# Performance work log

Measured on AMD Instinct MI355X. Metric: run time of the kernel, lower is better.

The kernel has to match this reference:

```python
import jax, jax.numpy as jnp
import numpy as np

DEG20 = 20.0 * np.pi / 180.0
MIN_PATCH_AREA = 4.0


def _bilinear(p, sy, sx):
    """Bilinear sample [P,P,3] patch at float coords sy,sx of shape [H,W]."""
    P = p.shape[0]
    y0 = jnp.floor(sy)
    x0 = jnp.floor(sx)
    wy = (sy - y0)[..., None]
    wx = (sx - x0)[..., None]
    y0i = jnp.clip(y0, 0, P - 1).astype(jnp.int32)
    y1i = jnp.clip(y0 + 1, 0, P - 1).astype(jnp.int32)
    x0i = jnp.clip(x0, 0, P - 1).astype(jnp.int32)
    x1i = jnp.clip(x0 + 1, 0, P - 1).astype(jnp.int32)
    v00 = p[y0i, x0i]
    v01 = p[y0i, x1i]
    v10 = p[y1i, x0i]
    v11 = p[y1i, x1i]
    return v00 * (1 - wy) * (1 - wx) + v01 * (1 - wy) * wx + v10 * wy * (1 - wx) + v11 * wy * wx


def setup_inputs() -> dict:
    key = jax.random.key(0)
    B, H, W, N, P = 16, 768, 768, 16, 640
    k_img, k_patch, k_ymin, k_xmin, k_h, k_w = jax.random.split(key, 6)
    images = jax.random.uniform(k_img, (B, H, W, 3), jnp.float32, -1.0, 1.0)
    patch = jax.random.uniform(k_patch, (P, P, 3), jnp.float32, -1.0, 1.0)
    ymin = jax.random.uniform(k_ymin, (B, N), jnp.float32, 0.0, 0.55 * H)
    xmin = jax.random.uniform(k_xmin, (B, N), jnp.float32, 0.0, 0.55 * W)
    bh = jax.random.uniform(k_h, (B, N), jnp.float32, 60.0, 0.40 * H)
    bw = jax.random.uniform(k_w, (B, N), jnp.float32, 60.0, 0.40 * W)
    ymax = jnp.minimum(ymin + bh, float(H))
    xmax = jnp.minimum(xmin + bw, float(W))
    boxes = jnp.stack([ymin, xmin, ymax, xmax], axis=-1)  # [B,N,4]
    scale = jnp.float32(0.4)
    return {"images": images, "boxes": boxes, "patch": patch, "scale": scale}


def reference(images, boxes, patch, scale):
    B, H, W, _ = images.shape
    P = patch.shape[0]
    Hf, Wf = jnp.float32(H), jnp.float32(W)
    yy = jnp.arange(H, dtype=jnp.float32)[:, None]  # [H,1]
    xx = jnp.arange(W, dtype=jnp.float32)[None, :]  # [1,W]
    scale_s = jnp.reshape(scale, ())

    def per_image(img, bxs, ikey):
        kw, kb, kboxes = jax.random.split(ikey, 3)
        # random_print_adjust: w*patch + b, clipped
        wmul = 0.5 + 0.1 * jax.random.normal(kw, (1, 1, 3), jnp.float32)
        badd = 0.01 * jax.random.normal(kb, (1, 1, 3), jnp.float32)
        p = jnp.clip(wmul * patch + badd, -1.0, 1.0)
        # brightness matcher: shift patch mean toward image mean
        p = jnp.clip(p + (jnp.mean(img) - jnp.mean(p)), -1.0, 1.0)
        bkeys = jax.random.split(kboxes, bxs.shape[0])

        def step(im, inp):
            box, bk = inp
            k1, k2, k3, k4, k5 = jax.random.split(bk, 5)
            ymin, xmin, ymax, xmax = box[0], box[1], box[2], box[3]
            bh = ymax - ymin
            bw = xmax - xmin
            longer = jnp.maximum(bh, bw)
            psize = jnp.floor(longer * scale_s)            # patch_h == patch_w
            diag = jnp.minimum(jnp.float32(np.sqrt(2.0)) * psize, Wf)
            tol = 0.2
            oy = ymin + bh / 2 + jax.random.uniform(k1, (), jnp.float32, -tol * bh / 2, tol * bh / 2)
            ox = xmin + bw / 2 + jax.random.uniform(k2, (), jnp.float32, -tol * bw / 2, tol * bw / 2)
            y0 = jnp.maximum(oy - diag / 2, 0.0)
            x0 = jnp.maximum(ox - diag / 2, 0.0)
            y0 = jnp.where(y0 + diag > Hf, Hf - diag, y0)
            x0 = jnp.where(x0 + diag > Wf, Wf - diag, x0)
            # TF casts to int32 (truncation; values >= 0 -> floor)
            y0 = jnp.floor(y0)
            x0 = jnp.floor(x0)
            d = jnp.floor(diag)
            ph = psize
            valid = (ph * ph) > MIN_PATCH_AREA
            top = jnp.floor((d - ph) / 2.0)                # pad offset
            angle = jax.random.uniform(k3, (), jnp.float32, -DEG20, DEG20)
            # pixel coords inside the diag x diag patch window
            u = yy - y0                                    # [H,1] -> broadcast [H,W]
            v = xx - x0
            inside = (u >= 0) & (u < d) & (v >= 0) & (v < d)
            c = (d - 1.0) / 2.0
            ca, sa = jnp.cos(angle), jnp.sin(angle)
            iu = c + ca * (u - c) - sa * (v - c)           # inverse rotation about center
            iv = c + sa * (u - c) + ca * (v - c)
            py = iu - top                                  # coords in resized patch
            px = iv - top
            # bilinear resize (half-pixel centers): src = (dst+0.5)*P/ph - 0.5
            sy = (py + 0.5) * (P / ph) - 0.5
            sx = (px + 0.5) * (P / ph) - 0.5
            val = _bilinear(p, sy, sx)                     # [H,W,3]
            noise = jax.random.uniform(k4, (H, W, 3), jnp.float32, -0.01, 0.01)
            delta = jax.random.uniform(k5, (), jnp.float32, -0.3, 0.3)
            val = jnp.clip(val + noise + delta, -1.0, 1.0)
            in_patch = (py >= 0) & (py <= ph - 1) & (px >= 0) & (px <= ph - 1)
            fill = jnp.where(in_patch[..., None], val, -2.0)  # pad/rotate fill = -2
            blended = jnp.clip(jnp.where(fill < -1.0, im, fill), -1.0, 1.0)
            write = inside[..., None] & valid
            return jnp.where(write, blended, im), None

        out, _ = jax.lax.scan(step, img, (bxs, bkeys))
        return out

    ikeys = jax.random.split(jax.random.key(42), B)
    return jax.vmap(per_image)(images, boxes, ikeys)
```

## Files before the change

### kernel.cpp

```cpp
#include <hip/hip_runtime.h>
#include <stdint.h>

#define NIMG 16
#define IMH 768
#define IMW 768
#define NBOX 16
#define PSZ 640
#define IMG_ELEMS (IMH*IMW*3)
#define PATCH_ELEMS (PSZ*PSZ*3)
#define CPBLK 128
#define PATBLK 64
#define RENDER_BLKS 4096

typedef float f4 __attribute__((ext_vector_type(4)));

__device__ __forceinline__ uint32_t rotl32(uint32_t v, int r){ return (v<<r)|(v>>(32-r)); }

__device__ __forceinline__ void threefry(uint32_t k0, uint32_t k1, uint32_t c0, uint32_t c1,
                                         uint32_t& o0, uint32_t& o1){
  uint32_t ks2 = k0 ^ k1 ^ 0x1BD11BDAu;
  uint32_t x0 = c0 + k0, x1 = c1 + k1;
#define TFR(r) { x0 += x1; x1 = rotl32(x1,(r)); x1 ^= x0; }
  TFR(13) TFR(15) TFR(26) TFR(6)
  x0 += k1;  x1 += ks2 + 1u;
  TFR(17) TFR(29) TFR(16) TFR(24)
  x0 += ks2; x1 += k0 + 2u;
  TFR(13) TFR(15) TFR(26) TFR(6)
  x0 += k0;  x1 += k1 + 3u;
  TFR(17) TFR(29) TFR(16) TFR(24)
  x0 += k1;  x1 += ks2 + 4u;
  TFR(13) TFR(15) TFR(26) TFR(6)
  x0 += ks2; x1 += k0 + 5u;
#undef TFR
  o0 = x0; o1 = x1;
}

__device__ __forceinline__ uint32_t rbits(uint32_t k0, uint32_t k1, uint32_t idx){
  uint32_t a, b; threefry(k0, k1, 0u, idx, a, b); return a ^ b;
}

__device__ __forceinline__ float u01(uint32_t bits){
  return __uint_as_float((bits >> 9) | 0x3f800000u) - 1.0f;
}

__device__ __forceinline__ float juniform(uint32_t k0, uint32_t k1, uint32_t idx, float mn, float mx){
  float u = u01(rbits(k0, k1, idx));
  float span = __fsub_rn(mx, mn);
  return fmaxf(mn, __fadd_rn(__fmul_rn(u, span), mn));
}

__device__ float erfinv32(float x){
  float w = -log1pf(-x*x);
  float p;
  if (w < 5.0f){
    w = w - 2.5f;
    p = 2.81022636e-08f;
    p = fmaf(p,w, 3.43273939e-07f);
    p = fmaf(p,w,-3.5233877e-06f);
    p = fmaf(p,w,-4.39150654e-06f);
    p = fmaf(p,w, 0.00021858087f);
    p = fmaf(p,w,-0.00125372503f);
    p = fmaf(p,w,-0.00417768164f);
    p = fmaf(p,w, 0.246640727f);
    p = fmaf(p,w, 1.50140941f);
  } else {
    w = sqrtf(w) - 3.0f;
    p = -0.000200214257f;
    p = fmaf(p,w, 0.000100950558f);
    p = fmaf(p,w, 0.00134934322f);
    p = fmaf(p,w,-0.00367342844f);
    p = fmaf(p,w, 0.00573950773f);
    p = fmaf(p,w,-0.0076224613f);
    p = fmaf(p,w, 0.00943887047f);
    p = fmaf(p,w, 1.00167406f);
    p = fmaf(p,w, 2.83297682f);
  }
  return p * x;
}

__device__ __forceinline__ void compute_wb(int b, float* rec){
  uint32_t i0,i1; threefry(0u, 42u, 0u, (uint32_t)b, i0, i1);
  uint32_t kw0,kw1; threefry(i0, i1, 0u, 0u, kw0, kw1);
  uint32_t kb0,kb1; threefry(i0, i1, 0u, 1u, kb0, kb1);
  const float lo = -0.99999994f;
  const float span = __fsub_rn(1.0f, lo);
  const float sq2 = 1.4142135623730951f;
  for (int j = 0; j < 3; j++){
    float uw = u01(rbits(kw0, kw1, (uint32_t)j));
    float rw = fmaxf(lo, __fadd_rn(__fmul_rn(uw, span), lo));
    float nw = __fmul_rn(sq2, erfinv32(rw));
    rec[j] = __fadd_rn(0.5f, __fmul_rn(0.1f, nw));
    float ub = u01(rbits(kb0, kb1, (uint32_t)j));
    float rb = fmaxf(lo, __fadd_rn(__fmul_rn(ub, span), lo));
    float nb = __fmul_rn(sq2, erfinv32(rb));
    rec[3+j] = __fmul_rn(0.01f, nb);
  }
  rec[6] = 0.0f; rec[7] = 0.0f;
}

__global__ __launch_bounds__(256) void k_front(const float* __restrict__ img,
                                               const float* __restrict__ patch,
                                               float* __restrict__ out,
                                               double* __restrict__ imgpart,
                                               double* __restrict__ patpart){
  if (blockIdx.x < PATBLK){
    __shared__ float wl[NIMG*8];
    if (threadIdx.x < NIMG) compute_wb(threadIdx.x, &wl[threadIdx.x*8]);
    __syncthreads();
    double s[NIMG];
    #pragma unroll
    for (int im = 0; im < NIMG; im++) s[im] = 0.0;
    const f4* p4 = (const f4*)patch;
    const int N4 = PATCH_ELEMS/4;
    for (int i = blockIdx.x*256 + threadIdx.x; i < N4; i += PATBLK*256){
      f4 v = __builtin_nontemporal_load(p4 + i);
      int c = (i << 2) % 3;
      #pragma unroll
      for (int q = 0; q < 4; q++){
        float pv = v[q];
        #pragma unroll
        for (int im = 0; im < NIMG; im++){
          float t = __fadd_rn(__fmul_rn(wl[im*8 + c], pv), wl[im*8 + 3 + c]);
          t = fminf(fmaxf(t, -1.0f), 1.0f);
          s[im] += (double)t;
        }
        c = (c == 2) ? 0 : c + 1;
      }
    }
    #pragma unroll
    for (int im = 0; im < NIMG; im++)
      for (int o = 32; o > 0; o >>= 1) s[im] += __shfl_down(s[im], o);
    __shared__ double red[4][NIMG];
    if ((threadIdx.x & 63) == 0){
      int w = threadIdx.x >> 6;
      #pragma unroll
      for (int im = 0; im < NIMG; im++) red[w][im] = s[im];
    }
    __syncthreads();
    if (threadIdx.x < NIMG){
      double t = red[0][threadIdx.x] + red[1][threadIdx.x] + red[2][threadIdx.x] + red[3][threadIdx.x];
      patpart[threadIdx.x*PATBLK + blockIdx.x] = t;
    }
  } else {
    int bi = blockIdx.x - PATBLK;
    int b = bi >> 7;
    int j = bi & (CPBLK-1);
    const f4* src = (const f4*)(img + (size_t)b * IMG_ELEMS);
    f4* dst = (f4*)(out + (size_t)b * IMG_ELEMS);
    const int N4 = IMG_ELEMS/4;
    double s = 0.0;
    for (int i = j*256 + threadIdx.x; i < N4; i += CPBLK*256){
      f4 v = __builtin_nontemporal_load(src + i);
      __builtin_nontemporal_store(v, dst + i);
      s += (double)v.x; s += (double)v.y; s += (double)v.z; s += (double)v.w;
    }
    for (int o = 32; o > 0; o >>= 1) s += __shfl_down(s, o);
    __shared__ double sm[4];
    if ((threadIdx.x & 63) == 0) sm[threadIdx.x >> 6] = s;
    __syncthreads();
    if (threadIdx.x == 0) imgpart[b*CPBLK + j] = sm[0]+sm[1]+sm[2]+sm[3];
  }
}

__global__ __launch_bounds__(256) void k_final(const double* __restrict__ imgpart,
                        const double* __restrict__ patpart,
                        float* __restrict__ shift, float* __restrict__ wbg,
                        float* __restrict__ boxp, int* __restrict__ chunkoff,
                        const float* __restrict__ boxes, const float* __restrict__ scale){
  int t = threadIdx.x;
  if (t < NIMG){
    double si = 0.0, sp = 0.0;
    for (int j = 0; j < CPBLK; j++) si += imgpart[t*CPBLK + j];
    for (int j = 0; j < PATBLK; j++) sp += patpart[t*PATBLK + j];
    float mi = (float)(si / (double)IMG_ELEMS);
    float mp = (float)(sp / (double)PATCH_ELEMS);
    shift[t] = __fsub_rn(mi, mp);
    compute_wb(t, &wbg[t*8]);
  }

  int nch = 0;
  {
    int b = t / NBOX, i = t % NBOX;
    uint32_t i0,i1;  threefry(0u, 42u, 0u, (uint32_t)b, i0, i1);
    uint32_t kx0,kx1; threefry(i0, i1, 0u, 2u, kx0, kx1);
    uint32_t bk0,bk1; threefry(kx0, kx1, 0u, (uint32_t)i, bk0, bk1);
    uint32_t K1a,K1b,K2a,K2b,K3a,K3b,K4a,K4b,K5a,K5b;
    threefry(bk0,bk1,0u,0u,K1a,K1b);
    threefry(bk0,bk1,0u,1u,K2a,K2b);
    threefry(bk0,bk1,0u,2u,K3a,K3b);
    threefry(bk0,bk1,0u,3u,K4a,K4b);
    threefry(bk0,bk1,0u,4u,K5a,K5b);

    const float* bx = boxes + (size_t)t*4;
    float ymin = bx[0], xmin = bx[1], ymax = bx[2], xmax = bx[3];
    float bh = __fsub_rn(ymax, ymin);
    float bw = __fsub_rn(xmax, xmin);
    float longer = fmaxf(bh, bw);
    float sc = scale[0];
    float psize = floorf(__fmul_rn(longer, sc));
    float diag = fminf(__fmul_rn(1.4142135623730951f, psize), 768.0f);

    float mny = __fdiv_rn(__fmul_rn(-0.2f, bh), 2.0f);
    float mxy = __fdiv_rn(__fmul_rn( 0.2f, bh), 2.0f);
    float r1 = juniform(K1a, K1b, 0u, mny, mxy);
    float oy = __fadd_rn(__fadd_rn(ymin, __fdiv_rn(bh, 2.0f)), r1);
    float mnx = __fdiv_rn(__fmul_rn(-0.2f, bw), 2.0f);
    float mxx = __fdiv_rn(__fmul_rn( 0.2f, bw), 2.0f);
    float r2 = juniform(K2a, K2b, 0u, mnx, mxx);
    float ox = __fadd_rn(__fadd_rn(xmin, __fdiv_rn(bw, 2.0f)), r2);

    float hd = __fdiv_rn(diag, 2.0f);
    float y0 = fmaxf(__fsub_rn(oy, hd), 0.0f);
    float x0 = fmaxf(__fsub_rn(ox, hd), 0.0f);
    if (__fadd_rn(y0, diag) > 768.0f) y0 = __fsub_rn(768.0f, diag);
    if (__fadd_rn(x0, diag) > 768.0f) x0 = __fsub_rn(768.0f, diag);
    y0 = floorf(y0);
    x0 = floorf(x0);
    float d  = floorf(diag);
    float ph = psize;
    float top = floorf(__fdiv_rn(__fsub_rn(d, ph), 2.0f));

    const float A20 = 0.3490658503988659f;
    float ang = juniform(K3a, K3b, 0u, -A20, A20);
    double da = (double)ang;
    float ca = (float)cos(da);
    float sa = (float)sin(da);
    float delta = juniform(K5a, K5b, 0u, -0.3f, 0.3f);
    float valid = (__fmul_rn(ph, ph) > 4.0f) ? 1.0f : 0.0f;
    float cc  = __fdiv_rn(__fsub_rn(d, 1.0f), 2.0f);
    float sres = __fdiv_rn(640.0f, ph);

    float* o = boxp + t*16;
    o[0]=y0; o[1]=x0; o[2]=d; o[3]=ph; o[4]=top; o[5]=cc; o[6]=ca; o[7]=sa;
    o[8]=sres; o[9]=delta;
    o[10]=__uint_as_float(K4a); o[11]=__uint_as_float(K4b);
    o[12]=valid; o[13]=__fsub_rn(ph, 1.0f); o[14]=0.0f; o[15]=0.0f;

    if (valid != 0.0f){
      int di = (int)d;
      nch = (di*di + 255) >> 8;
    }
  }

  __shared__ int scan[256];
  scan[t] = nch; __syncthreads();
  for (int off = 1; off < 256; off <<= 1){
    int v = (t >= off) ? scan[t-off] : 0;
    __syncthreads();
    scan[t] += v;
    __syncthreads();
  }
  if (t == 0) chunkoff[0] = 0;
  chunkoff[t+1] = scan[t];
}

__global__ __launch_bounds__(256) void k_render3(
    const float* __restrict__ patch, const float* __restrict__ wbg,
    const float* __restrict__ shiftg, const float* __restrict__ boxp,
    const int* __restrict__ chunkoff, float* __restrict__ out)
{
  __shared__ float sp[256*16];
  __shared__ float wl[NIMG*8];
  __shared__ float shl[NIMG];
  __shared__ int   coff[258];
  for (int i = threadIdx.x; i < 4096; i += 256) sp[i] = boxp[i];
  if (threadIdx.x < NIMG*8) wl[threadIdx.x] = wbg[threadIdx.x];
  if (threadIdx.x < NIMG)   shl[threadIdx.x] = shiftg[threadIdx.x];
  for (int i = threadIdx.x; i < 257; i += 256) coff[i] = chunkoff[i];
  __syncthreads();
  int total = coff[256];

  for (int chunk = blockIdx.x; chunk < total; chunk += RENDER_BLKS){
    int lo = 0, hi = 255;
    #pragma unroll
    for (int it = 0; it < 8; it++){
      int mid = (lo + hi + 1) >> 1;
      if (coff[mid] <= chunk) lo = mid; else hi = mid - 1;
    }
    int s = lo;
    const float* bp = &sp[s*16];
    int d = (int)bp[2];
    int dd = d*d;
    int idx = (chunk - coff[s])*256 + (int)threadIdx.x;
    if (idx >= dd) continue;

    int b = s >> 4, k = s & 15;
    float y0f = bp[0], x0f = bp[1];
    float cc = bp[5], ca = bp[6], sa = bp[7], top = bp[4];
    float ph1 = bp[13], sres = bp[8], delta = bp[9];

    int row = idx / d;
    int col = idx - row*d;
    int y = (int)y0f + row, x = (int)x0f + col;
    float yf = (float)y, xf = (float)x;
    float u = __fsub_rn(yf, y0f), v = __fsub_rn(xf, x0f);
    float um = __fsub_rn(u, cc), vm = __fsub_rn(v, cc);
    float iu = __fsub_rn(__fadd_rn(cc, __fmul_rn(ca, um)), __fmul_rn(sa, vm));
    float iv = __fadd_rn(__fadd_rn(cc, __fmul_rn(sa, um)), __fmul_rn(ca, vm));
    float py = __fsub_rn(iu, top), px = __fsub_rn(iv, top);
    if (!(py >= 0.0f && py <= ph1 && px >= 0.0f && px <= ph1)) continue;

    bool lose = false;
    for (int j = NBOX-1; j > k; --j){
      const float* bq = &sp[(b*NBOX + j)*16];
      if (bq[12] == 0.0f) continue;
      float u2 = __fsub_rn(yf, bq[0]);
      if (!(u2 >= 0.0f && u2 < bq[2])) continue;
      float v2 = __fsub_rn(xf, bq[1]);
      if (!(v2 >= 0.0f && v2 < bq[2])) continue;
      float um2 = __fsub_rn(u2, bq[5]), vm2 = __fsub_rn(v2, bq[5]);
      float iu2 = __fsub_rn(__fadd_rn(bq[5], __fmul_rn(bq[6], um2)), __fmul_rn(bq[7], vm2));
      float iv2 = __fadd_rn(__fadd_rn(bq[5], __fmul_rn(bq[7], um2)), __fmul_rn(bq[6], vm2));
      float py2 = __fsub_rn(iu2, bq[4]), px2 = __fsub_rn(iv2, bq[4]);
      if (py2 >= 0.0f && py2 <= bq[13] && px2 >= 0.0f && px2 <= bq[13]){ lose = true; break; }
    }
    if (lose) continue;

    float sy = __fsub_rn(__fmul_rn(__fadd_rn(py, 0.5f), sres), 0.5f);
    float sx = __fsub_rn(__fmul_rn(__fadd_rn(px, 0.5f), sres), 0.5f);
    float fy = floorf(sy), fx = floorf(sx);
    float wy = __fsub_rn(sy, fy), wx = __fsub_rn(sx, fx);
    int y0t = (int)fminf(fmaxf(fy, 0.0f), 639.0f);
    int y1t = (int)fminf(fmaxf(__fadd_rn(fy, 1.0f), 0.0f), 639.0f);
    int x0t = (int)fminf(fmaxf(fx, 0.0f), 639.0f);
    int x1t = (int)fminf(fmaxf(__fadd_rn(fx, 1.0f), 0.0f), 639.0f);
    float w00 = (1.0f-wy)*(1.0f-wx), w01 = (1.0f-wy)*wx;
    float w10 = wy*(1.0f-wx),        w11 = wy*wx;
    int i00 = (y0t*PSZ + x0t)*3, i01 = (y0t*PSZ + x1t)*3;
    int i10 = (y1t*PSZ + x0t)*3, i11 = (y1t*PSZ + x1t)*3;
    const float* wbb = &wl[b*8];
    float shf = shl[b];
    uint32_t n0 = __float_as_uint(bp[10]);
    uint32_t n1 = __float_as_uint(bp[11]);
    int pix = y*IMW + x;
    size_t base = (size_t)b*IMG_ELEMS + (size_t)pix*3;
    #pragma unroll
    for (int c = 0; c < 3; c++){
      float wm = wbb[c], bd = wbb[3+c];
      float v00 = fminf(fmaxf(__fadd_rn(__fmul_rn(wm, patch[i00+c]), bd), -1.0f), 1.0f);
      v00 = fminf(fmaxf(__fadd_rn(v00, shf), -1.0f), 1.0f);
      float v01 = fminf(fmaxf(__fadd_rn(__fmul_rn(wm, patch[i01+c]), bd), -1.0f), 1.0f);
      v01 = fminf(fmaxf(__fadd_rn(v01, shf), -1.0f), 1.0f);
      float v10 = fminf(fmaxf(__fadd_rn(__fmul_rn(wm, patch[i10+c]), bd), -1.0f), 1.0f);
      v10 = fminf(fmaxf(__fadd_rn(v10, shf), -1.0f), 1.0f);
      float v11 = fminf(fmaxf(__fadd_rn(__fmul_rn(wm, patch[i11+c]), bd), -1.0f), 1.0f);
      v11 = fminf(fmaxf(__fadd_rn(v11, shf), -1.0f), 1.0f);
      float val = v00*w00 + v01*w01 + v10*w10 + v11*w11;
      float un = u01(rbits(n0, n1, (uint32_t)(pix*3 + c)));
      float span = __fsub_rn(0.01f, -0.01f);
      float nz = fmaxf(-0.01f, __fadd_rn(__fmul_rn(un, span), -0.01f));
      val = __fadd_rn(__fadd_rn(val, nz), delta);
      out[base + c] = fminf(fmaxf(val, -1.0f), 1.0f);
    }
  }
}

extern "C" void kernel_launch(void* const* d_in, const int* in_sizes, int n_in,
                              void* d_out, int out_size, void* d_ws, size_t ws_size,
                              hipStream_t stream){
  (void)in_sizes; (void)n_in; (void)out_size; (void)ws_size;
  const float* images = (const float*)d_in[0];
  const float* boxes  = (const float*)d_in[1];
  const float* patch  = (const float*)d_in[2];
  const float* scale  = (const float*)d_in[3];
  float* out = (float*)d_out;

  char* ws = (char*)d_ws;
  double* imgpart = (double*)(ws);
  double* patpart = (double*)(ws + 16384);
  float*  wb      = (float*)(ws + 24576);
  float*  shift   = (float*)(ws + 25088);
  float*  boxp    = (float*)(ws + 25600);
  int*    chunkoff= (int*)(ws + 41984);

  hipLaunchKernelGGL(k_front,   dim3(PATBLK + NIMG*CPBLK), dim3(256), 0, stream,
                     images, patch, out, imgpart, patpart);
  hipLaunchKernelGGL(k_final,   dim3(1), dim3(256), 0, stream,
                     imgpart, patpart, shift, wb, boxp, chunkoff, boxes, scale);
  hipLaunchKernelGGL(k_render3, dim3(RENDER_BLKS), dim3(256), 0, stream,
                     patch, wb, shift, boxp, chunkoff, out);
}
```

Baseline: 139.3 us.

## Repack patch to padded float4 layout for vectorized bilinear gathers

Adds extra blocks in the front kernel that rewrite the RGB patch into an RGBA-padded float4 buffer in workspace, so the render kernel fetches each bilinear corner with one 16-byte load instead of three scalar loads. The padded path runs only when the workspace is large enough, otherwise it falls back to the old path. The image copy also switches from nontemporal to ordinary loads and stores and accumulates in float4 before converting to double. The final kernel now spreads its partial-sum reduction across 16 lanes per image. The changed summation order could shift the computed means slightly, and the padding adds a 6.5 MB extra write.

```diff
diff --git a/kernel.cpp b/kernel.cpp
--- a/kernel.cpp
+++ b/kernel.cpp
@@ -10,6 +10,7 @@
 #define PATCH_ELEMS (PSZ*PSZ*3)
 #define CPBLK 128
 #define PATBLK 64
+#define PADBLK 64
 #define RENDER_BLKS 4096
 
 typedef float f4 __attribute__((ext_vector_type(4)));
@@ -102,7 +103,8 @@
                                                const float* __restrict__ patch,
                                                float* __restrict__ out,
                                                double* __restrict__ imgpart,
-                                               double* __restrict__ patpart){
+                                               double* __restrict__ patpart,
+                                               f4* __restrict__ pad4, int do_pad){
   if (blockIdx.x < PATBLK){
     __shared__ float wl[NIMG*8];
     if (threadIdx.x < NIMG) compute_wb(threadIdx.x, &wl[threadIdx.x*8]);
@@ -113,7 +115,7 @@
     const f4* p4 = (const f4*)patch;
     const int N4 = PATCH_ELEMS/4;
     for (int i = blockIdx.x*256 + threadIdx.x; i < N4; i += PATBLK*256){
-      f4 v = __builtin_nontemporal_load(p4 + i);
+      f4 v = p4[i];
       int c = (i << 2) % 3;
       #pragma unroll
       for (int q = 0; q < 4; q++){
@@ -141,24 +143,39 @@
       double t = red[0][threadIdx.x] + red[1][threadIdx.x] + red[2][threadIdx.x] + red[3][threadIdx.x];
       patpart[threadIdx.x*PATBLK + blockIdx.x] = t;
     }
-  } else {
+  } else if (blockIdx.x < PATBLK + NIMG*CPBLK){
     int bi = blockIdx.x - PATBLK;
     int b = bi >> 7;
     int j = bi & (CPBLK-1);
     const f4* src = (const f4*)(img + (size_t)b * IMG_ELEMS);
     f4* dst = (f4*)(out + (size_t)b * IMG_ELEMS);
     const int N4 = IMG_ELEMS/4;
-    double s = 0.0;
+    f4 fs = {0.0f, 0.0f, 0.0f, 0.0f};
+    #pragma unroll 2
     for (int i = j*256 + threadIdx.x; i < N4; i += CPBLK*256){
-      f4 v = __builtin_nontemporal_load(src + i);
-      __builtin_nontemporal_store(v, dst + i);
-      s += (double)v.x; s += (double)v.y; s += (double)v.z; s += (double)v.w;
-    }
+      f4 v = src[i];
+      dst[i] = v;
+      fs += v;
+    }
+    double s = ((double)fs.x + (double)fs.y) + ((double)fs.z + (double)fs.w);
     for (int o = 32; o > 0; o >>= 1) s += __shfl_down(s, o);
     __shared__ double sm[4];
     if ((threadIdx.x & 63) == 0) sm[threadIdx.x >> 6] = s;
     __syncthreads();
     if (threadIdx.x == 0) imgpart[b*CPBLK + j] = sm[0]+sm[1]+sm[2]+sm[3];
+  } else {
+    if (!do_pad) return;
+    int pb = blockIdx.x - (PATBLK + NIMG*CPBLK);
+    const f4* src = (const f4*)patch;
+    const int NG = PSZ*PSZ/4;
+    for (int g = pb*256 + threadIdx.x; g < NG; g += PADBLK*256){
+      f4 a = src[g*3+0], b2 = src[g*3+1], c2 = src[g*3+2];
+      f4 t0 = {a.x,  a.y,  a.z,  0.0f};
+      f4 t1 = {a.w,  b2.x, b2.y, 0.0f};
+      f4 t2 = {b2.z, b2.w, c2.x, 0.0f};
+      f4 t3 = {c2.y, c2.z, c2.w, 0.0f};
+      pad4[g*4+0] = t0; pad4[g*4+1] = t1; pad4[g*4+2] = t2; pad4[g*4+3] = t3;
+    }
   }
 }
 
@@ -168,14 +185,21 @@
                         float* __restrict__ boxp, int* __restrict__ chunkoff,
                         const float* __restrict__ boxes, const float* __restrict__ scale){
   int t = threadIdx.x;
-  if (t < NIMG){
+  {
+    int im = t >> 4, l = t & 15;
     double si = 0.0, sp = 0.0;
-    for (int j = 0; j < CPBLK; j++) si += imgpart[t*CPBLK + j];
-    for (int j = 0; j < PATBLK; j++) sp += patpart[t*PATBLK + j];
-    float mi = (float)(si / (double)IMG_ELEMS);
-    float mp = (float)(sp / (double)PATCH_ELEMS);
-    shift[t] = __fsub_rn(mi, mp);
-    compute_wb(t, &wbg[t*8]);
+    #pragma unroll
+    for (int j = 0; j < CPBLK/16; j++) si += imgpart[im*CPBLK + l + j*16];
+    #pragma unroll
+    for (int j = 0; j < PATBLK/16; j++) sp += patpart[im*PATBLK + l + j*16];
+    #pragma unroll
+    for (int o = 8; o > 0; o >>= 1){ si += __shfl_down(si, o); sp += __shfl_down(sp, o); }
+    if (l == 0){
+      float mi = (float)(si / (double)IMG_ELEMS);
+      float mp = (float)(sp / (double)PATCH_ELEMS);
+      shift[im] = __fsub_rn(mi, mp);
+      compute_wb(im, &wbg[im*8]);
+    }
   }
 
   int nch = 0;
@@ -254,10 +278,12 @@
   chunkoff[t+1] = scan[t];
 }
 
+template<int USEPAD>
 __global__ __launch_bounds__(256) void k_render3(
-    const float* __restrict__ patch, const float* __restrict__ wbg,
-    const float* __restrict__ shiftg, const float* __restrict__ boxp,
-    const int* __restrict__ chunkoff, float* __restrict__ out)
+    const float* __restrict__ patch, const f4* __restrict__ pad4,
+    const float* __restrict__ wbg, const float* __restrict__ shiftg,
+    const float* __restrict__ boxp, const int* __restrict__ chunkoff,
+    float* __restrict__ out)
 {
   __shared__ float sp[256*16];
   __shared__ float wl[NIMG*8];
@@ -326,24 +352,36 @@
     int x1t = (int)fminf(fmaxf(__fadd_rn(fx, 1.0f), 0.0f), 639.0f);
     float w00 = (1.0f-wy)*(1.0f-wx), w01 = (1.0f-wy)*wx;
     float w10 = wy*(1.0f-wx),        w11 = wy*wx;
-    int i00 = (y0t*PSZ + x0t)*3, i01 = (y0t*PSZ + x1t)*3;
-    int i10 = (y1t*PSZ + x0t)*3, i11 = (y1t*PSZ + x1t)*3;
     const float* wbb = &wl[b*8];
     float shf = shl[b];
     uint32_t n0 = __float_as_uint(bp[10]);
     uint32_t n1 = __float_as_uint(bp[11]);
     int pix = y*IMW + x;
     size_t base = (size_t)b*IMG_ELEMS + (size_t)pix*3;
+
+    f4 p00, p01, p10, p11;
+    int i00, i01, i10, i11;
+    if constexpr (USEPAD){
+      p00 = pad4[y0t*PSZ + x0t]; p01 = pad4[y0t*PSZ + x1t];
+      p10 = pad4[y1t*PSZ + x0t]; p11 = pad4[y1t*PSZ + x1t];
+      i00 = i01 = i10 = i11 = 0;
+    } else {
+      i00 = (y0t*PSZ + x0t)*3; i01 = (y0t*PSZ + x1t)*3;
+      i10 = (y1t*PSZ + x0t)*3; i11 = (y1t*PSZ + x1t)*3;
+    }
     #pragma unroll
     for (int c = 0; c < 3; c++){
       float wm = wbb[c], bd = wbb[3+c];
-      float v00 = fminf(fmaxf(__fadd_rn(__fmul_rn(wm, patch[i00+c]), bd), -1.0f), 1.0f);
+      float t00, t01, t10, t11;
+      if constexpr (USEPAD){ t00 = p00[c]; t01 = p01[c]; t10 = p10[c]; t11 = p11[c]; }
+      else { t00 = patch[i00+c]; t01 = patch[i01+c]; t10 = patch[i10+c]; t11 = patch[i11+c]; }
+      float v00 = fminf(fmaxf(__fadd_rn(__fmul_rn(wm, t00), bd), -1.0f), 1.0f);
       v00 = fminf(fmaxf(__fadd_rn(v00, shf), -1.0f), 1.0f);
-      float v01 = fminf(fmaxf(__fadd_rn(__fmul_rn(wm, patch[i01+c]), bd), -1.0f), 1.0f);
+      float v01 = fminf(fmaxf(__fadd_rn(__fmul_rn(wm, t01), bd), -1.0f), 1.0f);
       v01 = fminf(fmaxf(__fadd_rn(v01, shf), -1.0f), 1.0f);
-      float v10 = fminf(fmaxf(__fadd_rn(__fmul_rn(wm, patch[i10+c]), bd), -1.0f), 1.0f);
+      float v10 = fminf(fmaxf(__fadd_rn(__fmul_rn(wm, t10), bd), -1.0f), 1.0f);
       v10 = fminf(fmaxf(__fadd_rn(v10, shf), -1.0f), 1.0f);
-      float v11 = fminf(fmaxf(__fadd_rn(__fmul_rn(wm, patch[i11+c]), bd), -1.0f), 1.0f);
+      float v11 = fminf(fmaxf(__fadd_rn(__fmul_rn(wm, t11), bd), -1.0f), 1.0f);
       v11 = fminf(fmaxf(__fadd_rn(v11, shf), -1.0f), 1.0f);
       float val = v00*w00 + v01*w01 + v10*w10 + v11*w11;
       float un = u01(rbits(n0, n1, (uint32_t)(pix*3 + c)));
@@ -358,7 +396,7 @@
 extern "C" void kernel_launch(void* const* d_in, const int* in_sizes, int n_in,
                               void* d_out, int out_size, void* d_ws, size_t ws_size,
                               hipStream_t stream){
-  (void)in_sizes; (void)n_in; (void)out_size; (void)ws_size;
+  (void)in_sizes; (void)n_in; (void)out_size;
   const float* images = (const float*)d_in[0];
   const float* boxes  = (const float*)d_in[1];
   const float* patch  = (const float*)d_in[2];
@@ -372,11 +410,20 @@
   float*  shift   = (float*)(ws + 25088);
   float*  boxp    = (float*)(ws + 25600);
   int*    chunkoff= (int*)(ws + 41984);
-
-  hipLaunchKernelGGL(k_front,   dim3(PATBLK + NIMG*CPBLK), dim3(256), 0, stream,
-                     images, patch, out, imgpart, patpart);
+  f4*     pad4    = (f4*)(ws + 65536);
+
+  size_t need = 65536 + (size_t)PSZ*PSZ*16;
+  int do_pad = (ws_size >= need) ? 1 : 0;
+
+  int front_blks = PATBLK + NIMG*CPBLK + (do_pad ? PADBLK : 0);
+  hipLaunchKernelGGL(k_front,   dim3(front_blks), dim3(256), 0, stream,
+                     images, patch, out, imgpart, patpart, pad4, do_pad);
   hipLaunchKernelGGL(k_final,   dim3(1), dim3(256), 0, stream,
                      imgpart, patpart, shift, wb, boxp, chunkoff, boxes, scale);
-  hipLaunchKernelGGL(k_render3, dim3(RENDER_BLKS), dim3(256), 0, stream,
-                     patch, wb, shift, boxp, chunkoff, out);
-}
+  if (do_pad)
+    hipLaunchKernelGGL(k_render3<1>, dim3(RENDER_BLKS), dim3(256), 0, stream,
+                       patch, pad4, wb, shift, boxp, chunkoff, out);
+  else
+    hipLaunchKernelGGL(k_render3<0>, dim3(RENDER_BLKS), dim3(256), 0, stream,
+                       patch, pad4, wb, shift, boxp, chunkoff, out);
+}
```

Measured after the change: 139.1 us. Within noise of the previous version (-0.2%).
